# Performance work log

Measured on AMD Instinct MI355X. Metric: run time of the kernel, lower is better.

## Reference

```python
import jax, jax.numpy as jnp
import numpy as np

N_EXPERTS = 64
LN_EPS = 1e-5


def _layer_norm(x, gamma, beta, eps=LN_EPS):
    mu = jnp.mean(x, axis=-1, keepdims=True)
    var = jnp.mean(jnp.square(x - mu), axis=-1, keepdims=True)
    return (x - mu) * jax.lax.rsqrt(var + eps) * gamma + beta


def setup_inputs() -> dict:
    key = jax.random.key(0)
    ks = jax.random.split(key, 4)
    B, T, D, Ff = 2, 1024, 512, 2048
    x = jax.random.normal(ks[0], (B, T, D), dtype=jnp.float32)
    hex_weights = jax.random.uniform(ks[1], (B, T, N_EXPERTS), dtype=jnp.float32)
    W_in = jax.random.normal(ks[2], (N_EXPERTS, Ff, D), dtype=jnp.float32) * (D ** -0.5)
    b_in = jnp.zeros((N_EXPERTS, Ff), dtype=jnp.float32)
    W_out = jax.random.normal(ks[3], (N_EXPERTS, D, Ff), dtype=jnp.float32) * (Ff ** -0.5)
    b_out = jnp.zeros((N_EXPERTS, D), dtype=jnp.float32)
    ln_gamma = jnp.ones((D,), dtype=jnp.float32)
    ln_beta = jnp.zeros((D,), dtype=jnp.float32)
    return {"x": x, "hex_weights": hex_weights, "W_in": W_in, "b_in": b_in,
            "W_out": W_out, "b_out": b_out, "ln_gamma": ln_gamma,
            "ln_beta": ln_beta, "top_k": 4}


def reference(x, hex_weights, W_in, b_in, W_out, b_out, ln_gamma, ln_beta, top_k):
    B, T, D = x.shape
    N = B * T
    x_n = _layer_norm(x, ln_gamma, ln_beta)

    # top-k routing; renormalize the selected weights (matches torch topk + sum-norm)
    top_w, top_idx = jax.lax.top_k(hex_weights, top_k)          # (B,T,k)
    top_w = top_w / (jnp.sum(top_w, axis=-1, keepdims=True) + 1e-8)

    x_flat = x_n.reshape(N, D)
    # Scatter the k normalized weights into a dense (N, 64) routing matrix.
    # Non-selected experts get weight 0, so a dense per-expert sweep computes
    # EXACTLY the same combined output as the per-token gather in the original.
    w_full = jnp.zeros((N, N_EXPERTS), dtype=x.dtype)
    w_full = w_full.at[jnp.arange(N)[:, None], top_idx.reshape(N, top_k)].set(
        top_w.reshape(N, top_k))

    def body(acc, e):
        W_in_e, b_in_e, W_out_e, b_out_e, we = e  # we: (N,)
        h = jax.nn.silu(x_flat @ W_in_e.T + b_in_e)            # (N, d_ff)
        acc = acc + we[:, None] * (h @ W_out_e.T + b_out_e)    # (N, D)
        return acc, None

    acc, _ = jax.lax.scan(body, jnp.zeros_like(x_flat),
                          (W_in, b_in, W_out, b_out, w_full.T))
    return acc.reshape(B, T, D)
```

## Files before the change

### kernel.cpp

```cpp
#include <hip/hip_runtime.h>

#define NTOK 2048
#define DD   512
#define FFD  2048
#define NE   64
#define KSEL 4
#define NPAIR (NTOK*KSEL)
#define BM 192
#define BK 64
#define MAX_TILES 128
#define HROWS (NPAIR + 256)

typedef short s16x8 __attribute__((ext_vector_type(8)));
typedef float f32x4 __attribute__((ext_vector_type(4)));

typedef const __attribute__((address_space(1))) char* gptr_t;
typedef __attribute__((address_space(3))) char* lptr_t;

static __device__ __forceinline__ unsigned short f2bf(float f) {
    unsigned int u = __builtin_bit_cast(unsigned int, f);
    u += 0x7FFFu + ((u >> 16) & 1u);
    return (unsigned short)(u >> 16);
}

static __device__ __forceinline__ void packwrite(char* base, int nn, int kb, float4 v) {
    unsigned int lo = (unsigned int)f2bf(v.x) | ((unsigned int)f2bf(v.y) << 16);
    unsigned int hi = (unsigned int)f2bf(v.z) | ((unsigned int)f2bf(v.w) << 16);
    *(uint2*)(base + nn * 128 + (kb ^ ((nn & 7) << 4))) = make_uint2(lo, hi);
}

__global__ __launch_bounds__(256) void k_ln_route(
    const float* __restrict__ x, const float* __restrict__ hw,
    const float* __restrict__ gamma, const float* __restrict__ beta,
    unsigned short* __restrict__ xn_bf, int* __restrict__ counts,
    int* __restrict__ tok_e, float* __restrict__ tok_w)
{
    const int t = blockIdx.x;
    const int tid = threadIdx.x;
    const float* xr = x + (size_t)t * DD;
    float v0 = xr[tid];
    float v1 = xr[tid + 256];
    float s = v0 + v1, s2 = v0*v0 + v1*v1;
    #pragma unroll
    for (int off = 32; off > 0; off >>= 1) {
        s  += __shfl_down(s, off);
        s2 += __shfl_down(s2, off);
    }
    __shared__ float rsum[4], rsum2[4];
    __shared__ float smu, srs;
    const int wid = tid >> 6, lane = tid & 63;
    if (lane == 0) { rsum[wid] = s; rsum2[wid] = s2; }
    __syncthreads();
    if (tid == 0) {
        float a = 0.f, b = 0.f;
        for (int i = 0; i < 4; ++i) { a += rsum[i]; b += rsum2[i]; }
        float mu  = a * (1.f / DD);
        float var = b * (1.f / DD) - mu * mu;
        smu = mu; srs = rsqrtf(var + 1e-5f);
    }
    __syncthreads();
    const float mu = smu, rstd = srs;
    xn_bf[(size_t)t*DD + tid]       = f2bf((v0 - mu) * rstd * gamma[tid]       + beta[tid]);
    xn_bf[(size_t)t*DD + tid + 256] = f2bf((v1 - mu) * rstd * gamma[tid + 256] + beta[tid + 256]);

    if (tid < 64) {
        float v = hw[(size_t)t*NE + tid];
        int   sel[KSEL]; float sw[KSEL];
        #pragma unroll
        for (int j = 0; j < KSEL; ++j) {
            float m = v; int mi = tid;
            #pragma unroll
            for (int off = 32; off > 0; off >>= 1) {
                float ov = __shfl_xor(m, off);
                int   oi = __shfl_xor(mi, off);
                if (ov > m || (ov == m && oi < mi)) { m = ov; mi = oi; }
            }
            if (tid == mi) v = -1e30f;
            sel[j] = mi; sw[j] = m;
        }
        if (tid == 0) {
            float ssum = sw[0] + sw[1] + sw[2] + sw[3];
            float inv = 1.f / (ssum + 1e-8f);
            #pragma unroll
            for (int j = 0; j < KSEL; ++j) {
                tok_e[t*KSEL + j] = sel[j];
                tok_w[t*KSEL + j] = sw[j] * inv;
                atomicAdd(&counts[sel[j]], 1);
            }
        }
    }
}

__global__ void k_scan(const int* __restrict__ counts, int* __restrict__ offs,
                       int* __restrict__ cursor, int* __restrict__ tile_e,
                       int* __restrict__ tile_r, int* __restrict__ ntiles)
{
    __shared__ int sc[NE], stc[NE];
    const int tid = threadIdx.x;
    sc[tid] = counts[tid];
    __syncthreads();
    int off = 0;
    for (int i = 0; i < tid; ++i) off += sc[i];
    offs[tid] = off; cursor[tid] = off;
    if (tid == NE-1) offs[NE] = off + sc[NE-1];
    int tc = (sc[tid] + BM - 1) / BM;
    stc[tid] = tc;
    __syncthreads();
    int toff = 0;
    for (int i = 0; i < tid; ++i) toff += stc[i];
    for (int j = 0; j < tc; ++j) { tile_e[toff + j] = tid; tile_r[toff + j] = off + j*BM; }
    if (tid == NE-1) *ntiles = toff + tc;
}

__global__ __launch_bounds__(256) void k_scatter(
    const int* __restrict__ tok_e, const float* __restrict__ tok_w,
    int* __restrict__ cursor, int* __restrict__ pair_tok,
    float* __restrict__ pair_w, int* __restrict__ inv)
{
    int i = blockIdx.x * 256 + threadIdx.x;
    if (i >= NPAIR) return;
    int t = i >> 2;
    int e = tok_e[i];
    int slot = atomicAdd(&cursor[e], 1);
    pair_tok[slot] = t;
    pair_w[slot] = tok_w[i];
    inv[i] = slot;
}

template<int KD, bool IS_IN, int BNX>
__global__ __launch_bounds__(256, 2) void k_moe_gemm(
    const unsigned short* __restrict__ Abf,
    const float* __restrict__ W, const float* __restrict__ bias,
    const int* __restrict__ tile_e, const int* __restrict__ tile_r,
    const int* __restrict__ ntiles, const int* __restrict__ offs,
    const int* __restrict__ pr_tok, const float* __restrict__ pr_w,
    unsigned short* __restrict__ Hout, float* __restrict__ Pout)
{
    constexpr int NK = KD / BK;
    constexpr int NB = BNX / 16;
    constexpr int MT = IS_IN ? 6 : 3;
    const int ti = blockIdx.x;
    if (ti >= *ntiles) return;
    const int e    = tile_e[ti];
    const int row0 = tile_r[ti];
    const int rend = offs[e + 1];
    const int n0   = blockIdx.y * BNX;
    const int NOUT = IS_IN ? FFD : DD;
    const float* __restrict__ Wb = W + (size_t)e * NOUT * KD;

    __shared__ __align__(16) unsigned short As[2 * BM * BK];
    __shared__ __align__(16) unsigned short Bs[2 * BNX * BK];

    const int tid  = threadIdx.x;
    const int lane = tid & 63, wave = tid >> 6;
    const int wmbase = IS_IN ? (wave >> 1) * 96 : wave * 48;
    const int wnbase = IS_IN ? (wave & 1) * 64 : 0;

    const char* asrc[6];
    #pragma unroll
    for (int i = 0; i < 6; ++i) {
        int seg  = wave * 6 + i;
        int r    = seg * 8 + (lane >> 3);
        int grow = row0 + r;
        int cg   = (lane & 7) ^ (r & 7);
        size_t rowbase;
        if (IS_IN) {
            int tok = (grow < rend) ? pr_tok[grow] : 0;
            rowbase = (size_t)tok * (KD * 2);
        } else {
            rowbase = (size_t)grow * (KD * 2);
        }
        asrc[i] = (const char*)Abf + rowbase + (size_t)cg * 16;
    }

    const float* wsrc0 = Wb + (size_t)(n0 + (tid >> 4)) * KD + (tid & 15) * 4;
    const int nb = tid >> 4;
    const int kb = (tid & 15) * 8;

    f32x4 acc[MT][4];
    #pragma unroll
    for (int m = 0; m < MT; ++m)
        #pragma unroll
        for (int n = 0; n < 4; ++n)
            acc[m][n] = (f32x4){0.f, 0.f, 0.f, 0.f};

    {
        #pragma unroll
        for (int i = 0; i < 6; ++i)
            __builtin_amdgcn_global_load_lds((gptr_t)asrc[i],
                (lptr_t)((char*)As + (wave * 6 + i) * 1024), 16, 0, 0);
        float4 breg[NB];
        #pragma unroll
        for (int i = 0; i < NB; ++i)
            breg[i] = *(const float4*)(wsrc0 + (size_t)i * 16 * KD);
        #pragma unroll
        for (int i = 0; i < NB; ++i)
            packwrite((char*)Bs, nb + i * 16, kb, breg[i]);
    }
    __syncthreads();

    int buf = 0;
    for (int kt = 0; kt < NK; ++kt) {
        const int k0n = (kt + 1) * BK;
        float4 bregN[NB];
        if (kt + 1 < NK) {
            #pragma unroll
            for (int i = 0; i < 6; ++i)
                __builtin_amdgcn_global_load_lds((gptr_t)(asrc[i] + (size_t)k0n * 2),
                    (lptr_t)((char*)As + (buf ^ 1) * (BM * BK * 2) + (wave * 6 + i) * 1024),
                    16, 0, 0);
            #pragma unroll
            for (int i = 0; i < NB; ++i)
                bregN[i] = *(const float4*)(wsrc0 + (size_t)i * 16 * KD + k0n);
        }
        __builtin_amdgcn_sched_barrier(0);

        const char* Ab = (const char*)As + buf * (BM * BK * 2);
        const char* Bb = (const char*)Bs + buf * (BNX * BK * 2);
        #pragma unroll
        for (int h = 0; h < 2; ++h) {
            s16x8 af[MT], bfr[4];
            const int koff = h * 64 + (lane >> 4) * 16;
            #pragma unroll
            for (int m = 0; m < MT; ++m) {
                int row = wmbase + m * 16 + (lane & 15);
                af[m] = *(const s16x8*)(Ab + row * 128 + (koff ^ ((row & 7) << 4)));
            }
            #pragma unroll
            for (int n = 0; n < 4; ++n) {
                int row = wnbase + n * 16 + (lane & 15);
                bfr[n] = *(const s16x8*)(Bb + row * 128 + (koff ^ ((row & 7) << 4)));
            }
            #pragma unroll
            for (int m = 0; m < MT; ++m)
                #pragma unroll
                for (int n = 0; n < 4; ++n)
                    acc[m][n] = __builtin_amdgcn_mfma_f32_16x16x32_bf16(af[m], bfr[n], acc[m][n], 0, 0, 0);
        }
        __builtin_amdgcn_sched_barrier(0);

        if (kt + 1 < NK) {
            char* Bw = (char*)Bs + (buf ^ 1) * (BNX * BK * 2);
            #pragma unroll
            for (int i = 0; i < NB; ++i)
                packwrite(Bw, nb + i * 16, kb, bregN[i]);
        }
        __syncthreads();
        buf ^= 1;
    }

    #pragma unroll
    for (int m = 0; m < MT; ++m) {
        #pragma unroll
        for (int r = 0; r < 4; ++r) {
            int row = row0 + wmbase + m * 16 + (lane >> 4) * 4 + r;
            if (row < rend) {
                if (IS_IN) {
                    #pragma unroll
                    for (int n = 0; n < 4; ++n) {
                        int f = n0 + wnbase + n * 16 + (lane & 15);
                        float v = acc[m][n][r] + bias[e * FFD + f];
                        v = v / (1.f + __expf(-v));
                        Hout[(size_t)row * FFD + f] = f2bf(v);
                    }
                } else {
                    float pw = pr_w[row];
                    #pragma unroll
                    for (int n = 0; n < 4; ++n) {
                        int d = n0 + wnbase + n * 16 + (lane & 15);
                        Pout[(size_t)row * DD + d] = (acc[m][n][r] + bias[e * DD + d]) * pw;
                    }
                }
            }
        }
    }
}

__global__ __launch_bounds__(128) void k_combine(
    const float* __restrict__ pout, const int* __restrict__ inv,
    float* __restrict__ out)
{
    const int t = blockIdx.x;
    const int tid = threadIdx.x;
    const float4* p0 = (const float4*)(pout + (size_t)inv[t*4+0]*DD);
    const float4* p1 = (const float4*)(pout + (size_t)inv[t*4+1]*DD);
    const float4* p2 = (const float4*)(pout + (size_t)inv[t*4+2]*DD);
    const float4* p3 = (const float4*)(pout + (size_t)inv[t*4+3]*DD);
    float4 a = p0[tid], b = p1[tid], c = p2[tid], d = p3[tid];
    float4 r;
    r.x = a.x + b.x + c.x + d.x;
    r.y = a.y + b.y + c.y + d.y;
    r.z = a.z + b.z + c.z + d.z;
    r.w = a.w + b.w + c.w + d.w;
    ((float4*)(out + (size_t)t*DD))[tid] = r;
}

extern "C" void kernel_launch(void* const* d_in, const int* in_sizes, int n_in,
                              void* d_out, int out_size, void* d_ws, size_t ws_size,
                              hipStream_t stream)
{
    const float* x     = (const float*)d_in[0];
    const float* hw    = (const float*)d_in[1];
    const float* Win   = (const float*)d_in[2];
    const float* bin   = (const float*)d_in[3];
    const float* Wout  = (const float*)d_in[4];
    const float* bout  = (const float*)d_in[5];
    const float* gamma = (const float*)d_in[6];
    const float* beta  = (const float*)d_in[7];
    float* out = (float*)d_out;

    char* ws = (char*)d_ws;
    size_t o = 0;
    unsigned short* xn_bf = (unsigned short*)(ws + o); o += (size_t)NTOK * DD * 2;
    unsigned short* H     = (unsigned short*)(ws + o); o += (size_t)HROWS * FFD * 2;
    float* pout   = (float*)(ws + o); o += (size_t)NPAIR * DD * 4;
    int*   counts = (int*)(ws + o);   o += 256;
    int*   offs   = (int*)(ws + o);   o += 512;
    int*   cursor = (int*)(ws + o);   o += 256;
    int*   tok_e  = (int*)(ws + o);   o += (size_t)NPAIR * 4;
    float* tok_w  = (float*)(ws + o); o += (size_t)NPAIR * 4;
    int*   inv    = (int*)(ws + o);   o += (size_t)NPAIR * 4;
    int*   pr_tok = (int*)(ws + o);   o += (size_t)NPAIR * 4;
    float* pr_w   = (float*)(ws + o); o += (size_t)NPAIR * 4;
    int*   tile_e = (int*)(ws + o);   o += 512;
    int*   tile_r = (int*)(ws + o);   o += 512;
    int*   ntiles = (int*)(ws + o);   o += 256;
    (void)ws_size; (void)in_sizes; (void)n_in; (void)out_size;

    hipMemsetAsync(counts, 0, 256, stream);
    k_ln_route<<<dim3(NTOK), dim3(256), 0, stream>>>(x, hw, gamma, beta, xn_bf, counts, tok_e, tok_w);
    k_scan<<<dim3(1), dim3(64), 0, stream>>>(counts, offs, cursor, tile_e, tile_r, ntiles);
    k_scatter<<<dim3(NPAIR/256), dim3(256), 0, stream>>>(tok_e, tok_w, cursor, pr_tok, pr_w, inv);

    dim3 gA(MAX_TILES, FFD / 128);
    k_moe_gemm<DD, true, 128><<<gA, dim3(256), 0, stream>>>(
        xn_bf, Win, bin, tile_e, tile_r, ntiles, offs, pr_tok, pr_w, H, nullptr);
    dim3 gB(MAX_TILES, DD / 64);
    k_moe_gemm<FFD, false, 64><<<gB, dim3(256), 0, stream>>>(
        H, Wout, bout, tile_e, tile_r, ntiles, offs, pr_tok, pr_w, nullptr, pout);

    k_combine<<<dim3(NTOK), dim3(128), 0, stream>>>(pout, inv, out);
}
```

Baseline: 242.8 us.

## Deepen weight prefetch to two stages with manual waitcnt and flatten grid

Restructures the MoE GEMM main loop so fp32 weight tiles are prefetched two k-steps ahead into alternating register sets, using explicit s_waitcnt vmcnt counts and raw s_barrier instead of __syncthreads. This keeps more global loads in flight to hide weight-load latency. The grid becomes 1D with tiles in the low bits, so blocks for the same N-slice are dispatched together and are more likely to reuse weights in cache. Padding rows now gather a real token of the tile instead of token 0. The hand-set wait counts are fragile and assume a fixed number of outstanding loads per step.

```diff
diff --git a/kernel.cpp b/kernel.cpp
--- a/kernel.cpp
+++ b/kernel.cpp
@@ -139,12 +139,13 @@
     constexpr int NK = KD / BK;
     constexpr int NB = BNX / 16;
     constexpr int MT = IS_IN ? 6 : 3;
-    const int ti = blockIdx.x;
+    const int ti = blockIdx.x & (MAX_TILES - 1);
+    const int yg = blockIdx.x >> 7;
     if (ti >= *ntiles) return;
     const int e    = tile_e[ti];
     const int row0 = tile_r[ti];
     const int rend = offs[e + 1];
-    const int n0   = blockIdx.y * BNX;
+    const int n0   = yg * BNX;
     const int NOUT = IS_IN ? FFD : DD;
     const float* __restrict__ Wb = W + (size_t)e * NOUT * KD;
 
@@ -165,7 +166,7 @@
         int cg   = (lane & 7) ^ (r & 7);
         size_t rowbase;
         if (IS_IN) {
-            int tok = (grow < rend) ? pr_tok[grow] : 0;
+            int tok = (grow < rend) ? pr_tok[grow] : pr_tok[row0];
             rowbase = (size_t)tok * (KD * 2);
         } else {
             rowbase = (size_t)grow * (KD * 2);
@@ -184,70 +185,100 @@
         for (int n = 0; n < 4; ++n)
             acc[m][n] = (f32x4){0.f, 0.f, 0.f, 0.f};
 
-    {
-        #pragma unroll
-        for (int i = 0; i < 6; ++i)
-            __builtin_amdgcn_global_load_lds((gptr_t)asrc[i],
-                (lptr_t)((char*)As + (wave * 6 + i) * 1024), 16, 0, 0);
-        float4 breg[NB];
-        #pragma unroll
-        for (int i = 0; i < NB; ++i)
-            breg[i] = *(const float4*)(wsrc0 + (size_t)i * 16 * KD);
-        #pragma unroll
-        for (int i = 0; i < NB; ++i)
-            packwrite((char*)Bs, nb + i * 16, kb, breg[i]);
-    }
-    __syncthreads();
+    float4 bset0[NB], bset1[NB];
+
+    #pragma unroll
+    for (int i = 0; i < 6; ++i)
+        __builtin_amdgcn_global_load_lds((gptr_t)asrc[i],
+            (lptr_t)((char*)As + (wave * 6 + i) * 1024), 16, 0, 0);
+    #pragma unroll
+    for (int i = 0; i < NB; ++i)
+        bset0[i] = *(const float4*)(wsrc0 + (size_t)i * 16 * KD);
+    #pragma unroll
+    for (int i = 0; i < NB; ++i)
+        bset1[i] = *(const float4*)(wsrc0 + (size_t)i * 16 * KD + BK);
+    if constexpr (NB == 8) asm volatile("s_waitcnt vmcnt(8)" ::: "memory");
+    else                   asm volatile("s_waitcnt vmcnt(4)" ::: "memory");
+    __builtin_amdgcn_sched_barrier(0);
+    #pragma unroll
+    for (int i = 0; i < NB; ++i)
+        packwrite((char*)Bs, nb + i * 16, kb, bset0[i]);
 
     int buf = 0;
-    for (int kt = 0; kt < NK; ++kt) {
-        const int k0n = (kt + 1) * BK;
-        float4 bregN[NB];
-        if (kt + 1 < NK) {
-            #pragma unroll
-            for (int i = 0; i < 6; ++i)
-                __builtin_amdgcn_global_load_lds((gptr_t)(asrc[i] + (size_t)k0n * 2),
-                    (lptr_t)((char*)As + (buf ^ 1) * (BM * BK * 2) + (wave * 6 + i) * 1024),
-                    16, 0, 0);
-            #pragma unroll
-            for (int i = 0; i < NB; ++i)
-                bregN[i] = *(const float4*)(wsrc0 + (size_t)i * 16 * KD + k0n);
-        }
-        __builtin_amdgcn_sched_barrier(0);
-
-        const char* Ab = (const char*)As + buf * (BM * BK * 2);
-        const char* Bb = (const char*)Bs + buf * (BNX * BK * 2);
-        #pragma unroll
-        for (int h = 0; h < 2; ++h) {
-            s16x8 af[MT], bfr[4];
-            const int koff = h * 64 + (lane >> 4) * 16;
-            #pragma unroll
-            for (int m = 0; m < MT; ++m) {
-                int row = wmbase + m * 16 + (lane & 15);
-                af[m] = *(const s16x8*)(Ab + row * 128 + (koff ^ ((row & 7) << 4)));
-            }
-            #pragma unroll
-            for (int n = 0; n < 4; ++n) {
-                int row = wnbase + n * 16 + (lane & 15);
-                bfr[n] = *(const s16x8*)(Bb + row * 128 + (koff ^ ((row & 7) << 4)));
-            }
-            #pragma unroll
-            for (int m = 0; m < MT; ++m)
-                #pragma unroll
-                for (int n = 0; n < 4; ++n)
-                    acc[m][n] = __builtin_amdgcn_mfma_f32_16x16x32_bf16(af[m], bfr[n], acc[m][n], 0, 0, 0);
-        }
-        __builtin_amdgcn_sched_barrier(0);
-
-        if (kt + 1 < NK) {
-            char* Bw = (char*)Bs + (buf ^ 1) * (BNX * BK * 2);
-            #pragma unroll
-            for (int i = 0; i < NB; ++i)
-                packwrite(Bw, nb + i * 16, kb, bregN[i]);
-        }
-        __syncthreads();
-        buf ^= 1;
-    }
+
+#define GEMM_STEP(KT, SUSE, SISS)                                                        \
+    {                                                                                    \
+        if ((KT) == NK - 1) {                                                            \
+            asm volatile("s_waitcnt vmcnt(0) lgkmcnt(0)" ::: "memory");                  \
+        } else if constexpr (NB == 8) {                                                  \
+            asm volatile("s_waitcnt vmcnt(8) lgkmcnt(0)" ::: "memory");                  \
+        } else {                                                                         \
+            asm volatile("s_waitcnt vmcnt(4) lgkmcnt(0)" ::: "memory");                  \
+        }                                                                                \
+        __builtin_amdgcn_s_barrier();                                                    \
+        __builtin_amdgcn_sched_barrier(0);                                               \
+        const int nbuf_ = buf ^ 1;                                                       \
+        if ((KT) + 1 < NK) {                                                             \
+            _Pragma("unroll")                                                            \
+            for (int i = 0; i < 6; ++i)                                                  \
+                __builtin_amdgcn_global_load_lds(                                        \
+                    (gptr_t)(asrc[i] + (size_t)((KT) + 1) * BK * 2),                     \
+                    (lptr_t)((char*)As + nbuf_ * (BM * BK * 2) + (wave * 6 + i) * 1024), \
+                    16, 0, 0);                                                           \
+        }                                                                                \
+        if ((KT) + 2 < NK) {                                                             \
+            _Pragma("unroll")                                                            \
+            for (int i = 0; i < NB; ++i)                                                 \
+                SISS[i] = *(const float4*)(wsrc0 + (size_t)i * 16 * KD + ((KT) + 2) * BK); \
+        }                                                                                \
+        __builtin_amdgcn_sched_barrier(0);                                               \
+        {                                                                                \
+            const char* Ab = (const char*)As + buf * (BM * BK * 2);                      \
+            const char* Bb = (const char*)Bs + buf * (BNX * BK * 2);                     \
+            _Pragma("unroll")                                                            \
+            for (int h = 0; h < 2; ++h) {                                                \
+                s16x8 af[MT], bfr[4];                                                    \
+                const int koff = h * 64 + (lane >> 4) * 16;                              \
+                _Pragma("unroll")                                                        \
+                for (int m = 0; m < MT; ++m) {                                           \
+                    int row = wmbase + m * 16 + (lane & 15);                             \
+                    af[m] = *(const s16x8*)(Ab + row * 128 + (koff ^ ((row & 7) << 4))); \
+                }                                                                        \
+                _Pragma("unroll")                                                        \
+                for (int n = 0; n < 4; ++n) {                                            \
+                    int row = wnbase + n * 16 + (lane & 15);                             \
+                    bfr[n] = *(const s16x8*)(Bb + row * 128 + (koff ^ ((row & 7) << 4)));\
+                }                                                                        \
+                _Pragma("unroll")                                                        \
+                for (int m = 0; m < MT; ++m)                                             \
+                    _Pragma("unroll")                                                    \
+                    for (int n = 0; n < 4; ++n)                                          \
+                        acc[m][n] = __builtin_amdgcn_mfma_f32_16x16x32_bf16(             \
+                            af[m], bfr[n], acc[m][n], 0, 0, 0);                          \
+            }                                                                            \
+        }                                                                                \
+        __builtin_amdgcn_sched_barrier(0);                                               \
+        if ((KT) + 1 < NK) {                                                             \
+            if ((KT) + 2 < NK) {                                                         \
+                if constexpr (NB == 8) asm volatile("s_waitcnt vmcnt(14)" ::: "memory"); \
+                else                   asm volatile("s_waitcnt vmcnt(10)" ::: "memory"); \
+            } else {                                                                     \
+                asm volatile("s_waitcnt vmcnt(6)" ::: "memory");                         \
+            }                                                                            \
+            __builtin_amdgcn_sched_barrier(0);                                           \
+            char* Bw = (char*)Bs + nbuf_ * (BNX * BK * 2);                               \
+            _Pragma("unroll")                                                            \
+            for (int i = 0; i < NB; ++i)                                                 \
+                packwrite(Bw, nb + i * 16, kb, SUSE[i]);                                 \
+        }                                                                                \
+        buf ^= 1;                                                                        \
+    }
+
+    for (int kt = 0; kt < NK; kt += 2) {
+        GEMM_STEP(kt,     bset1, bset0);
+        GEMM_STEP(kt + 1, bset0, bset1);
+    }
+#undef GEMM_STEP
 
     #pragma unroll
     for (int m = 0; m < MT; ++m) {
@@ -332,11 +363,9 @@
     k_scan<<<dim3(1), dim3(64), 0, stream>>>(counts, offs, cursor, tile_e, tile_r, ntiles);
     k_scatter<<<dim3(NPAIR/256), dim3(256), 0, stream>>>(tok_e, tok_w, cursor, pr_tok, pr_w, inv);
 
-    dim3 gA(MAX_TILES, FFD / 128);
-    k_moe_gemm<DD, true, 128><<<gA, dim3(256), 0, stream>>>(
+    k_moe_gemm<DD, true, 128><<<dim3(MAX_TILES * (FFD/128)), dim3(256), 0, stream>>>(
         xn_bf, Win, bin, tile_e, tile_r, ntiles, offs, pr_tok, pr_w, H, nullptr);
-    dim3 gB(MAX_TILES, DD / 64);
-    k_moe_gemm<FFD, false, 64><<<gB, dim3(256), 0, stream>>>(
+    k_moe_gemm<FFD, false, 64><<<dim3(MAX_TILES * (DD/64)), dim3(256), 0, stream>>>(
         H, Wout, bout, tile_e, tile_r, ntiles, offs, pr_tok, pr_w, nullptr, pout);
 
     k_combine<<<dim3(NTOK), dim3(128), 0, stream>>>(pout, inv, out);
```

Result: slower. 290.2 us (+19.5%).
